# Kernel optimization log

Measured on AMD Instinct MI355X. Metric: run time of the kernel, lower is better.

## Reference

```python
import jax, jax.numpy as jnp
import numpy as np

THRESHOLD = 1.25
CURRENT_DECAY = 0.25
VOLTAGE_DECAY = 0.03
SPIKE_PROB = 0.2


def setup_inputs() -> dict:
    key = jax.random.key(0)
    k1, k2 = jax.random.split(key)
    B, N, T = 2048, 16, 1024
    # binary input spike trains [batch, neurons, time]
    spike = (jax.random.uniform(k1, (B, N, T)) < SPIKE_PROB).astype(jnp.float32)
    # Dense synapse weight [out, in], no bias (lava-dl Dense default)
    W = jax.random.normal(k2, (N, N), dtype=jnp.float32) / np.sqrt(N)
    return {"spike": spike, "W": W}


def _cuba_dense(spike, W):
    # synaptic current input per timestep: z[b,o,t]
    z = jnp.einsum('oi,bit->bot', W, spike)
    zt = jnp.moveaxis(z, -1, 0)  # [T, B, O] for scan over time

    def step(carry, x):
        c, v = carry
        c = c * (1.0 - CURRENT_DECAY) + x
        v = v * (1.0 - VOLTAGE_DECAY) + c
        s = (v >= THRESHOLD).astype(v.dtype)
        v = v * (1.0 - s)  # hard reset to zero on spike
        return (c, v), s

    zero = jnp.zeros_like(zt[0])
    _, s = jax.lax.scan(step, (zero, zero), zt)  # s: [T, B, O]
    return jnp.moveaxis(s, 0, -1)  # [B, O, T]


def reference(spike, W):
    y = _cuba_dense(spike, W)  # [B, O, T] binary spikes
    # log-cosh free energy: exp(sum_neurons log(2 cosh(y))) -> [B, T]
    return jnp.exp(jnp.sum(jnp.log(2.0 * jnp.cosh(y)), axis=1))
```

## Files before the change

kernel.cpp:

```cpp
#include <hip/hip_runtime.h>
#include <stdint.h>

#define T_STEPS 1024
#define NWORDS  256
#define NB      8
#define SCAN_BLOCK (NB * 16)

typedef float f32x4 __attribute__((ext_vector_type(4)));

__global__ __launch_bounds__(256) void k_maskify(const float* __restrict__ spike,
                                                 unsigned long long* __restrict__ masks,
                                                 const float* __restrict__ W,
                                                 double* __restrict__ tab,
                                                 int B) {
    const int b  = blockIdx.x;
    const int tc = threadIdx.x;
    if (b < B) {
        const float4* sp = reinterpret_cast<const float4*>(spike) + (size_t)b * (16 * NWORDS);
        unsigned int m0 = 0, m1 = 0, m2 = 0, m3 = 0;
#pragma unroll
        for (int i = 0; i < 16; ++i) {
            float4 v = sp[i * NWORDS + tc];
            m0 |= (v.x >= 0.5f) ? (1u << i) : 0u;
            m1 |= (v.y >= 0.5f) ? (1u << i) : 0u;
            m2 |= (v.z >= 0.5f) ? (1u << i) : 0u;
            m3 |= (v.w >= 0.5f) ? (1u << i) : 0u;
        }
        masks[(size_t)b * NWORDS + tc] =
            (unsigned long long)m0 | ((unsigned long long)m1 << 16) |
            ((unsigned long long)m2 << 32) | ((unsigned long long)m3 << 48);
    } else {
        const int o = tc & 15;
        double w[16];
#pragma unroll
        for (int j = 0; j < 16; ++j) w[j] = (double)W[o * 16 + j];
#pragma unroll
        for (int k = 0; k < 32; ++k) {
            const int e    = tc + k * 256;
            const int byte = (e >> 4) & 255;
            const int s    = k >> 4;
            double slo = 0.0, shi = 0.0;
#pragma unroll
            for (int j = 0; j < 4; ++j) slo += (byte & (1 << j))  ? w[8 * s + j]     : 0.0;
#pragma unroll
            for (int j = 0; j < 4; ++j) shi += (byte & (16 << j)) ? w[8 * s + 4 + j] : 0.0;
            tab[s * 4096 + byte * 16 + o] = slo + shi;
        }
    }
}

__global__ __launch_bounds__(SCAN_BLOCK, 1) void k_scan(const double* __restrict__ tab,
                                                        const unsigned long long* __restrict__ masks,
                                                        float* __restrict__ out) {
    const int tid = threadIdx.x;
    const int bb  = tid >> 4;
    const int o   = tid & 15;
    const int b   = blockIdx.x * NB + bb;

    const uint64_t tb     = (uint64_t)tab;
    const uint64_t mb     = (uint64_t)masks;
    const uint64_t ob_out = (uint64_t)out;
    const uint32_t ob0    = (uint32_t)(o * 8);
    const uint32_t ob1    = ob0 + 32768u;
    const uint32_t vb_m   = (uint32_t)(b * (NWORDS * 8));
    const uint32_t vb_out = (uint32_t)(b * (T_STEPS * 4));
    const int grp_sh      = tid & 48;
    const bool writer     = (o == 0);

    double c = 0.0, v = 0.0;

    double T0_0, T0_1, T0_2, T0_3, T0_4, T0_5, T0_6, T0_7;
    double T1_0, T1_1, T1_2, T1_3, T1_4, T1_5, T1_6, T1_7;
    double T2_0, T2_1, T2_2, T2_3, T2_4, T2_5, T2_6, T2_7;
    double T3_0, T3_1, T3_2, T3_3, T3_4, T3_5, T3_6, T3_7;
    unsigned long long MA, MB, MC, MD, q0, q1;

#define GLT(DST, VOFF) \
    asm volatile("global_load_dwordx2 %0, %1, %2" : "=v"(DST) : "v"(VOFF), "s"(tb) : "memory")
#define GLM(DST, IDX) do { int _mi = (IDX); if (_mi > 255) _mi = 255;                 \
    const uint32_t _vo = vb_m + ((uint32_t)_mi << 3);                                 \
    asm volatile("global_load_dwordx2 %0, %1, %2" : "=v"(DST) : "v"(_vo), "s"(mb) : "memory"); } while (0)
#define WAITV(N) asm volatile("s_waitcnt vmcnt(" #N ")" ::: "memory")
#define SBAR __builtin_amdgcn_sched_barrier(0)

#define TISSUE(P, MW) do {                                                            \
    const uint32_t _lo = (uint32_t)(MW), _hi = (uint32_t)((MW) >> 32);                \
    uint32_t _a;                                                                      \
    _a = ob0 + ((_lo & 255u) << 7);          GLT(P##_0, _a);                          \
    _a = ob1 + (((_lo >> 8) & 255u) << 7);   GLT(P##_1, _a);                          \
    _a = ob0 + (((_lo >> 16) & 255u) << 7);  GLT(P##_2, _a);                          \
    _a = ob1 + ((_lo >> 24) << 7);           GLT(P##_3, _a);                          \
    _a = ob0 + ((_hi & 255u) << 7);          GLT(P##_4, _a);                          \
    _a = ob1 + (((_hi >> 8) & 255u) << 7);   GLT(P##_5, _a);                          \
    _a = ob0 + (((_hi >> 16) & 255u) << 7);  GLT(P##_6, _a);                          \
    _a = ob1 + ((_hi >> 24) << 7);           GLT(P##_7, _a);                          \
} while (0)

#define ZSTEP(ZL, ZH, OWEL) do {                                                      \
    const double _z = (ZL) + (ZH);                                                    \
    c = fma(c, 0.75, _z);                                                             \
    v = fma(v, 0.97, c);                                                              \
    const bool _s = (v >= 1.25);                                                      \
    const unsigned long long _bal = __ballot(_s);                                     \
    v = _s ? 0.0 : v;                                                                 \
    const uint32_t _k = __popc((uint32_t)(_bal >> grp_sh) & 0xFFFFu);                 \
    OWEL = exp2f(fmaf((float)_k, 0.62581400f, 16.0f));                                \
} while (0)

#define COMPUTE(P, WD) do {                                                           \
    f32x4 _ow;                                                                        \
    ZSTEP(P##_0, P##_1, _ow.x);                                                       \
    ZSTEP(P##_2, P##_3, _ow.y);                                                       \
    ZSTEP(P##_4, P##_5, _ow.z);                                                       \
    ZSTEP(P##_6, P##_7, _ow.w);                                                       \
    if (writer) {                                                                     \
        const uint32_t _vo = vb_out + ((uint32_t)(WD) << 4);                          \
        asm volatile("global_store_dwordx4 %0, %1, %2"                                \
                     :: "v"(_vo), "v"(_ow), "s"(ob_out) : "memory");                  \
    }                                                                                 \
} while (0)

#define BODY(WD, P, MU, MI) do {                                                      \
    GLM(MI, (WD) + 6);                                                                \
    WAITV(20); SBAR;                                                                  \
    COMPUTE(P, WD);                                                                   \
    TISSUE(P, MU); SBAR;                                                              \
} while (0)

    asm volatile("s_waitcnt vmcnt(0) lgkmcnt(0)" ::: "memory");

    GLM(q0, 0); GLM(q1, 1); GLM(MA, 2); GLM(MB, 3); GLM(MC, 4); GLM(MD, 5);
    WAITV(2); SBAR;
    TISSUE(T0, q0);
    TISSUE(T1, q1);
    TISSUE(T2, MA);
    TISSUE(T3, MB); SBAR;

    for (int w = 0; w < 252; w += 4) {
        BODY(w,     T0, MC, MA);
        BODY(w + 1, T1, MD, MB);
        BODY(w + 2, T2, MA, MC);
        BODY(w + 3, T3, MB, MD);
    }

    COMPUTE(T0, 252);
    WAITV(21); SBAR;
    COMPUTE(T1, 253);
    WAITV(12); SBAR;
    COMPUTE(T2, 254);
    WAITV(3); SBAR;
    COMPUTE(T3, 255);
    asm volatile("s_waitcnt vmcnt(0)" ::: "memory");

#undef GLT
#undef GLM
#undef WAITV
#undef SBAR
#undef TISSUE
#undef ZSTEP
#undef COMPUTE
#undef BODY
}

__global__ __launch_bounds__(SCAN_BLOCK) void k_scan_fb(const float* __restrict__ W,
                                                        const float* __restrict__ spike,
                                                        float* __restrict__ out) {
    __shared__ double ztab[4][16][16];
    __shared__ unsigned long long mlds[NB][NWORDS];
    __shared__ float outtab[17];
    const int tid = threadIdx.x, bb = tid >> 4, o = tid & 15;
    for (int e = tid; e < 4 * 16 * 16; e += SCAN_BLOCK) {
        const int oo = e & 15, idx = (e >> 4) & 15, seg = e >> 8;
        double s = 0.0;
#pragma unroll
        for (int j = 0; j < 4; ++j)
            if (idx & (1 << j)) s += (double)W[oo * 16 + seg * 4 + j];
        ztab[seg][idx][oo] = s;
    }
    if (tid < 17) {
        const double ln2 = 0.69314718055994530941723212145818;
        const double l2c1 = log(2.0 * cosh(1.0));
        outtab[tid] = (float)exp((16.0 - (double)tid) * ln2 + (double)tid * l2c1);
    }
    {
        const int part = tid & 15;
        const float4* spb = reinterpret_cast<const float4*>(spike) +
                            (size_t)(blockIdx.x * NB + bb) * (16 * NWORDS);
        for (int w = 0; w < 16; ++w) {
            const int tc = part * 16 + w;
            unsigned int m0 = 0, m1 = 0, m2 = 0, m3 = 0;
#pragma unroll
            for (int i = 0; i < 16; ++i) {
                float4 v = spb[i * NWORDS + tc];
                m0 |= (v.x >= 0.5f) ? (1u << i) : 0u;
                m1 |= (v.y >= 0.5f) ? (1u << i) : 0u;
                m2 |= (v.z >= 0.5f) ? (1u << i) : 0u;
                m3 |= (v.w >= 0.5f) ? (1u << i) : 0u;
            }
            mlds[bb][tc] = (unsigned long long)m0 | ((unsigned long long)m1 << 16) |
                           ((unsigned long long)m2 << 32) | ((unsigned long long)m3 << 48);
        }
    }
    __syncthreads();
    double c = 0.0, v = 0.0;
    const int b = blockIdx.x * NB + bb;
    float* outp = out + (size_t)b * T_STEPS;
    const int grp_sh = tid & 48;
    const bool writer = (o == 0);
    for (int tg = 0; tg < NWORDS; ++tg) {
        const unsigned long long mw = mlds[bb][tg];
#pragma unroll
        for (int j = 0; j < 4; ++j) {
            const unsigned int m = (unsigned int)(mw >> (16 * j)) & 0xFFFFu;
            const double z = (ztab[0][m & 15][o] + ztab[1][(m >> 4) & 15][o]) +
                             (ztab[2][(m >> 8) & 15][o] + ztab[3][(m >> 12) & 15][o]);
            c = fma(c, 0.75, z);
            v = fma(v, 0.97, c);
            const bool s = (v >= 1.25);
            const unsigned long long bal = __ballot(s);
            v = s ? 0.0 : v;
            if (writer) outp[tg * 4 + j] = outtab[(int)__popcll((bal >> grp_sh) & 0xFFFFull)];
        }
    }
}

extern "C" void kernel_launch(void* const* d_in, const int* in_sizes, int n_in,
                              void* d_out, int out_size, void* d_ws, size_t ws_size,
                              hipStream_t stream) {
    const float* spike = (const float*)d_in[0];
    const float* W     = (const float*)d_in[1];
    float* out         = (float*)d_out;

    const int B = in_sizes[0] / (16 * T_STEPS);

    const size_t mask_bytes = (size_t)B * NWORDS * sizeof(unsigned long long);
    const size_t tab_bytes  = 2 * 256 * 16 * sizeof(double);

    if (ws_size >= mask_bytes + tab_bytes) {
        unsigned long long* masks = (unsigned long long*)d_ws;
        double* tab = (double*)((char*)d_ws + mask_bytes);
        k_maskify<<<B + 1, 256, 0, stream>>>(spike, masks, W, tab, B);
        k_scan<<<B / NB, SCAN_BLOCK, 0, stream>>>(tab, masks, out);
    } else {
        k_scan_fb<<<B / NB, SCAN_BLOCK, 0, stream>>>(W, spike, out);
    }
}
```

Measured before the change: 91.94 us.

## Split scan into four time segments with redundant prefix recomputation

Launches four blocks per batch group. Each block recomputes the recurrence from t=0 up to the end of its own segment and stores only its segment's outputs to the real buffer; earlier outputs go to a workspace dump buffer. Launch bounds now allow two blocks per CU. This adds more concurrent blocks but does about 2.5x the total scan work. The longest segment still runs the full 1024 steps, so the serial critical path is not shortened, and extra blocks compete for memory bandwidth.

After: 168.1 us. 82.9% more time.

```diff
diff --git a/kernel.cpp b/kernel.cpp
--- a/kernel.cpp
+++ b/kernel.cpp
@@ -5,6 +5,7 @@
 #define NWORDS  256
 #define NB      8
 #define SCAN_BLOCK (NB * 16)
+#define NSEG    4
 
 typedef float f32x4 __attribute__((ext_vector_type(4)));
 
@@ -49,17 +50,24 @@
     }
 }
 
-__global__ __launch_bounds__(SCAN_BLOCK, 1) void k_scan(const double* __restrict__ tab,
+__global__ __launch_bounds__(SCAN_BLOCK, 2) void k_scan(const double* __restrict__ tab,
                                                         const unsigned long long* __restrict__ masks,
-                                                        float* __restrict__ out) {
+                                                        float* __restrict__ out,
+                                                        float* __restrict__ dump) {
     const int tid = threadIdx.x;
     const int bb  = tid >> 4;
     const int o   = tid & 15;
-    const int b   = blockIdx.x * NB + bb;
+    const int seg = blockIdx.x & (NSEG - 1);
+    const int blk = blockIdx.x >> 2;
+    const int b   = blk * NB + bb;
+
+    const int nw    = 64 * seg + 64;
+    const int wout0 = 64 * seg;
 
     const uint64_t tb     = (uint64_t)tab;
     const uint64_t mb     = (uint64_t)masks;
     const uint64_t ob_out = (uint64_t)out;
+    const uint64_t db_out = (uint64_t)dump;
     const uint32_t ob0    = (uint32_t)(o * 8);
     const uint32_t ob1    = ob0 + 32768u;
     const uint32_t vb_m   = (uint32_t)(b * (NWORDS * 8));
@@ -114,9 +122,10 @@
     ZSTEP(P##_4, P##_5, _ow.z);                                                       \
     ZSTEP(P##_6, P##_7, _ow.w);                                                       \
     if (writer) {                                                                     \
+        const uint64_t _sb = ((WD) >= wout0) ? ob_out : db_out;                       \
         const uint32_t _vo = vb_out + ((uint32_t)(WD) << 4);                          \
         asm volatile("global_store_dwordx4 %0, %1, %2"                                \
-                     :: "v"(_vo), "v"(_ow), "s"(ob_out) : "memory");                  \
+                     :: "v"(_vo), "v"(_ow), "s"(_sb) : "memory");                     \
     }                                                                                 \
 } while (0)
 
@@ -136,20 +145,21 @@
     TISSUE(T2, MA);
     TISSUE(T3, MB); SBAR;
 
-    for (int w = 0; w < 252; w += 4) {
+    for (int w = 0; w < nw - 4; w += 4) {
         BODY(w,     T0, MC, MA);
         BODY(w + 1, T1, MD, MB);
         BODY(w + 2, T2, MA, MC);
         BODY(w + 3, T3, MB, MD);
     }
 
-    COMPUTE(T0, 252);
+    const int e0 = nw - 4;
+    COMPUTE(T0, e0);
     WAITV(21); SBAR;
-    COMPUTE(T1, 253);
+    COMPUTE(T1, e0 + 1);
     WAITV(12); SBAR;
-    COMPUTE(T2, 254);
+    COMPUTE(T2, e0 + 2);
     WAITV(3); SBAR;
-    COMPUTE(T3, 255);
+    COMPUTE(T3, e0 + 3);
     asm volatile("s_waitcnt vmcnt(0)" ::: "memory");
 
 #undef GLT
@@ -235,12 +245,14 @@
 
     const size_t mask_bytes = (size_t)B * NWORDS * sizeof(unsigned long long);
     const size_t tab_bytes  = 2 * 256 * 16 * sizeof(double);
-
-    if (ws_size >= mask_bytes + tab_bytes) {
+    const size_t dump_bytes = (size_t)B * T_STEPS * sizeof(float);
+
+    if (ws_size >= mask_bytes + tab_bytes + dump_bytes) {
         unsigned long long* masks = (unsigned long long*)d_ws;
         double* tab = (double*)((char*)d_ws + mask_bytes);
+        float* dump = (float*)((char*)d_ws + mask_bytes + tab_bytes);
         k_maskify<<<B + 1, 256, 0, stream>>>(spike, masks, W, tab, B);
-        k_scan<<<B / NB, SCAN_BLOCK, 0, stream>>>(tab, masks, out);
+        k_scan<<<(B / NB) * NSEG, SCAN_BLOCK, 0, stream>>>(tab, masks, out, dump);
     } else {
         k_scan_fb<<<B / NB, SCAN_BLOCK, 0, stream>>>(W, spike, out);
     }
```
